# Performance work log

Hardware: AMD Instinct MI355X
Metric: run time of the kernel (lower is better)

The kernel has to match this reference:

```python
import jax, jax.numpy as jnp
import numpy as np

NUM_GRAPHS = 1024  # number of graphs in the batch (readout segments)


def setup_inputs() -> dict:
    key = jax.random.key(0)
    ks = jax.random.split(key, 10)
    N, F_IN, F1, F2, E = 100000, 64, 128, 64, 3200000
    x = jax.random.normal(ks[0], (N, F_IN), dtype=jnp.float32)
    adj = jax.random.randint(ks[1], (2, E), 0, N, dtype=jnp.int64)
    batch = jnp.sort(jax.random.randint(ks[2], (N,), 0, NUM_GRAPHS, dtype=jnp.int64))
    def xavier(k, shape):
        fan_in, fan_out = shape
        lim = jnp.sqrt(6.0 / (fan_in + fan_out))
        return jax.random.uniform(k, shape, jnp.float32, -lim, lim)
    W1 = xavier(ks[3], (F_IN, F1)); b1 = jax.random.uniform(ks[4], (F1,), jnp.float32)
    W2 = xavier(ks[5], (F1, F2));  b2 = jax.random.uniform(ks[6], (F2,), jnp.float32)
    Wm = xavier(ks[7], (2 * F2, F2)); bm = jax.random.uniform(ks[8], (F2,), jnp.float32)
    return {"x": x, "adj": adj, "batch": batch,
            "W1": W1, "b1": b1, "W2": W2, "b2": b2, "Wm": Wm, "bm": bm}


def _gcn_conv(x, W, b, src, dst):
    # GCNConv: out = D^{-1/2} (A + I) D^{-1/2} X W + b
    N = x.shape[0]
    h = x @ W  # [N, F_out]
    loops = jnp.arange(N, dtype=src.dtype)
    src_a = jnp.concatenate([src, loops])  # add self-loops
    dst_a = jnp.concatenate([dst, loops])
    deg = jax.ops.segment_sum(jnp.ones(src_a.shape[0], h.dtype), dst_a, num_segments=N)
    dinv = jax.lax.rsqrt(deg)  # deg >= 1 due to self-loops
    norm = dinv[src_a] * dinv[dst_a]  # [E+N]
    msg = h[src_a] * norm[:, None]    # gather + scale (memory-bound)
    return jax.ops.segment_sum(msg, dst_a, num_segments=N) + b


def _readout_meanmax(x, batch):
    G = NUM_GRAPHS
    s = jax.ops.segment_sum(x, batch, num_segments=G)
    cnt = jax.ops.segment_sum(jnp.ones(x.shape[0], x.dtype), batch, num_segments=G)
    mean = s / jnp.maximum(cnt, 1.0)[:, None]
    mx = jax.ops.segment_max(x, batch, num_segments=G)
    return jnp.concatenate([mean, mx], axis=1)  # [G, 2*F2]


def reference(x, adj, batch, W1, b1, W2, b2, Wm, bm):
    src, dst = adj[0], adj[1]
    h = jax.nn.relu(_gcn_conv(x, W1, b1, src, dst))
    h = _gcn_conv(h, W2, b2, src, dst)
    r = _readout_meanmax(h, batch)
    return r @ Wm + bm
```

## Files before the change

kernel.cpp:

```cpp
#include <hip/hip_runtime.h>
#include <hip/hip_fp16.h>
#include <cstdint>
#include <cstddef>

#define NGRAPH 1024
#define CHUNK 8192
#define SCTHREADS 512
#define SCIT (CHUNK / SCTHREADS)
#define MAXB 512
#define CAP 16384
#define WIDE 2048

typedef _Float16 f16x8 __attribute__((ext_vector_type(8)));
typedef float f32x4 __attribute__((ext_vector_type(4)));
typedef float f32x2 __attribute__((ext_vector_type(2)));


__global__ __launch_bounds__(SCTHREADS) void scatter1_kernel(const int* __restrict__ src,
        const int* __restrict__ dst, int E, int B,
        int* __restrict__ bcnt, unsigned* __restrict__ ebuck) {
    __shared__ unsigned sorted[CHUNK];
    __shared__ int h[MAXB];
    __shared__ int lo[MAXB];
    __shared__ int cur[MAXB];
    __shared__ int gbase[MAXB];
    __shared__ int wsum[8];
    int blk = blockIdx.x, tid = threadIdx.x;
    int base = blk * CHUNK;
    int cnt_i = E - base; if (cnt_i > CHUNK) cnt_i = CHUNK;

    h[tid] = 0;
    __syncthreads();

    unsigned rd[SCIT], rs[SCIT];
    #pragma unroll
    for (int it = 0; it < SCIT; ++it) {
        int i = base + tid + it * SCTHREADS;
        if (i < E) {
            rd[it] = (unsigned)dst[i];
            rs[it] = (unsigned)src[i];
            atomicAdd(&h[rd[it] >> 8], 1);
        } else rd[it] = 0xFFFFFFFFu;
    }
    __syncthreads();

    int hv = h[tid];
    if (tid < B) gbase[tid] = hv ? atomicAdd(&bcnt[tid], hv) : 0;

    int lane = tid & 63, wv = tid >> 6;
    int val = hv;
    #pragma unroll
    for (int o = 1; o < 64; o <<= 1) {
        int t = __shfl_up(val, o, 64);
        if (lane >= o) val += t;
    }
    if (lane == 63) wsum[wv] = val;
    __syncthreads();
    if (tid == 0) {
        int run = 0;
        #pragma unroll
        for (int i = 0; i < 8; ++i) { int t = wsum[i]; wsum[i] = run; run += t; }
    }
    __syncthreads();
    int excl = wsum[wv] + val - hv;
    lo[tid] = excl;
    cur[tid] = excl;
    __syncthreads();

    #pragma unroll
    for (int it = 0; it < SCIT; ++it) {
        if (rd[it] != 0xFFFFFFFFu) {
            int b = rd[it] >> 8;
            int p = atomicAdd(&cur[b], 1);
            sorted[p] = ((rd[it] & 255u) << 24) | rs[it];
        }
    }
    __syncthreads();

    for (int j = tid; j < cnt_i; j += SCTHREADS) {
        int l = (int)(((long long)j * B) / cnt_i);
        if (l > B - 1) l = B - 1;
        while (lo[l] > j) --l;
        while (l + 1 < B && lo[l + 1] <= j) ++l;
        ebuck[(size_t)l * CAP + gbase[l] + (j - lo[l])] = sorted[j];
    }
}

__global__ __launch_bounds__(256) void fine_kernel(const unsigned* __restrict__ ebuck,
        const int* __restrict__ bcnt, int N, int B,
        int* __restrict__ row_beg, int* __restrict__ row_end, float* __restrict__ dinv,
        int* __restrict__ esrc) {
    __shared__ int hcnt[256];
    __shared__ int loff[256];
    __shared__ int wsum[4];
    int b = blockIdx.x, tid = threadIdx.x;
    int beg = b * CAP;
    int cnt = bcnt[b];
    hcnt[tid] = 0;
    __syncthreads();
    {
        int e = tid;
        for (; e + 768 < cnt; e += 1024) {
            unsigned u0 = ebuck[beg + e];
            unsigned u1 = ebuck[beg + e + 256];
            unsigned u2 = ebuck[beg + e + 512];
            unsigned u3 = ebuck[beg + e + 768];
            atomicAdd(&hcnt[u0 >> 24], 1);
            atomicAdd(&hcnt[u1 >> 24], 1);
            atomicAdd(&hcnt[u2 >> 24], 1);
            atomicAdd(&hcnt[u3 >> 24], 1);
        }
        for (; e < cnt; e += 256)
            atomicAdd(&hcnt[ebuck[beg + e] >> 24], 1);
    }
    __syncthreads();
    int v = hcnt[tid];
    int n = (b << 8) + tid;
    int vp = (v + 15) & ~15;
    if (vp < 48) vp = 48;
    if (n >= N) vp = 0;

    int lane = tid & 63, wv = tid >> 6;
    int val = vp;
    #pragma unroll
    for (int o = 1; o < 64; o <<= 1) {
        int t = __shfl_up(val, o, 64);
        if (lane >= o) val += t;
    }
    if (lane == 63) wsum[wv] = val;
    __syncthreads();
    if (tid == 0) {
        int run = 0;
        #pragma unroll
        for (int i = 0; i < 4; ++i) { int t = wsum[i]; wsum[i] = run; run += t; }
    }
    __syncthreads();
    int excl = wsum[wv] + val - vp;

    float d = rsqrtf((float)(v + 1));
    if (n < N) {
        row_beg[n] = beg + excl;
        row_end[n] = beg + excl + vp;
        dinv[n] = d;
    }
    loff[tid] = excl;
    __syncthreads();
    {
        int e = tid;
        for (; e + 768 < cnt; e += 1024) {
            unsigned u0 = ebuck[beg + e];
            unsigned u1 = ebuck[beg + e + 256];
            unsigned u2 = ebuck[beg + e + 512];
            unsigned u3 = ebuck[beg + e + 768];
            int p0 = atomicAdd(&loff[u0 >> 24], 1);
            esrc[beg + p0] = (int)(u0 & 0xFFFFFF);
            int p1 = atomicAdd(&loff[u1 >> 24], 1);
            esrc[beg + p1] = (int)(u1 & 0xFFFFFF);
            int p2 = atomicAdd(&loff[u2 >> 24], 1);
            esrc[beg + p2] = (int)(u2 & 0xFFFFFF);
            int p3 = atomicAdd(&loff[u3 >> 24], 1);
            esrc[beg + p3] = (int)(u3 & 0xFFFFFF);
        }
        for (; e < cnt; e += 256) {
            unsigned u = ebuck[beg + e];
            int p = atomicAdd(&loff[u >> 24], 1);
            esrc[beg + p] = (int)(u & 0xFFFFFF);
        }
    }
    for (int p = excl + v; p < excl + vp; ++p) esrc[beg + p] = N;
}

__global__ __launch_bounds__(256) void pack_kernel(const float* __restrict__ x,
        const float* __restrict__ dinv, int N, unsigned char* __restrict__ xs) {
    int j = blockIdx.x * 256 + threadIdx.x;
    int total = N * 16;
    int stride = gridDim.x * 256;
    const float4* xr = (const float4*)x;
    for (; j < total; j += stride) {
        int node = j >> 4, cc = j & 15;
        float dd = dinv[node];
        float4 vv = xr[(size_t)node * 16 + cc];
        int lo2 = __builtin_amdgcn_cvt_pk_fp8_f32(vv.x * dd, vv.y * dd, 0, false);
        int hi2 = __builtin_amdgcn_cvt_pk_fp8_f32(vv.z * dd, vv.w * dd, 0, false);
        ((unsigned*)xs)[(size_t)node * 16 + cc] =
            (unsigned)(lo2 & 0xffff) | ((unsigned)(hi2 & 0xffff) << 16);
    }
}

__global__ __launch_bounds__(256) void prep_kernel(const float* __restrict__ W1,
        const float* __restrict__ W2, __half* __restrict__ W1s, __half* __restrict__ W2s,
        const int* __restrict__ batch, int N, int* __restrict__ goff,
        int* __restrict__ bcnt, unsigned char* __restrict__ xsq,
        unsigned char* __restrict__ tsq, float* __restrict__ zbias) {
    int t = threadIdx.x;
    if (blockIdx.x == 0) {
        #pragma unroll
        for (int it = 0; it < 4; ++it) {
            int s = t + it * 256;
            int n = s & 15, q = (s >> 4) & 3, nt = (s >> 6) & 7, ks = s >> 9;
            int k0 = ks * 32 + q * 8, col = nt * 16 + n;
            __align__(16) __half h[8];
            #pragma unroll
            for (int j = 0; j < 8; ++j) h[j] = (__half)W1[(k0 + j) * 128 + col];
            *((uint4*)&W1s[(size_t)s * 8]) = *(uint4*)h;
        }
        #pragma unroll
        for (int it = 0; it < 4; ++it) {
            int s = t + it * 256;
            int n = s & 15, q = (s >> 4) & 3, n2 = (s >> 6) & 3, ks2 = s >> 8;
            int k0 = ks2 * 32 + q * 8, col = n2 * 16 + n;
            __align__(16) __half h[8];
            #pragma unroll
            for (int j = 0; j < 8; ++j) h[j] = (__half)W2[(k0 + j) * 64 + col];
            *((uint4*)&W2s[(size_t)s * 8]) = *(uint4*)h;
        }
        uint4 z; z.x = 0; z.y = 0; z.z = 0; z.w = 0;
        if (t < 4)
            ((uint4*)(xsq + (size_t)N * 64))[t] = z;
        if (t < 4)
            ((uint4*)(tsq + (size_t)N * 64))[t] = z;
        if (t < 64) zbias[t] = 0.f;
    } else {
        int g = (blockIdx.x - 1) * 256 + t;
        if (g < MAXB) bcnt[g] = 0;
        if (g > NGRAPH) return;
        if (g == NGRAPH) { goff[g] = N; return; }
        int lo = 0, hi = N;
        while (lo < hi) {
            int mid = (lo + hi) >> 1;
            if (batch[mid] < g) lo = mid + 1; else hi = mid;
        }
        goff[g] = lo;
    }
}

__device__ __forceinline__ void acc8q(f32x2* a, const uint2& u) {
    a[0] += __builtin_amdgcn_cvt_pk_f32_fp8(u.x, false);
    a[1] += __builtin_amdgcn_cvt_pk_f32_fp8(u.x, true);
    a[2] += __builtin_amdgcn_cvt_pk_f32_fp8(u.y, false);
    a[3] += __builtin_amdgcn_cvt_pk_f32_fp8(u.y, true);
}

__device__ __forceinline__ void agg_core_q(const uint2* __restrict__ ts2,
        const int* __restrict__ esrc, int beg, int endp, int n, int g, int c,
        float* a) {
    f32x2 h0[4] = {}, h1[4] = {};
    if (g == 0) acc8q(h0, ts2[(size_t)n * 8 + c]);
    int U = (endp - beg) >> 3;
    int e0 = beg + g * U;
    if (U == 6) {
        int2 p0 = *(const int2*)&esrc[e0];
        int2 p1 = *(const int2*)&esrc[e0 + 2];
        int2 p2 = *(const int2*)&esrc[e0 + 4];
        uint2 u0 = ts2[(size_t)p0.x * 8 + c];
        uint2 u1 = ts2[(size_t)p0.y * 8 + c];
        uint2 u2 = ts2[(size_t)p1.x * 8 + c];
        uint2 u3 = ts2[(size_t)p1.y * 8 + c];
        uint2 u4 = ts2[(size_t)p2.x * 8 + c];
        uint2 u5 = ts2[(size_t)p2.y * 8 + c];
        acc8q(h0, u0); acc8q(h1, u1); acc8q(h0, u2); acc8q(h1, u3);
        acc8q(h0, u4); acc8q(h1, u5);
    } else if (U > 0) {
        for (int j = 0; j < U; j += 2) {
            int2 p = *(const int2*)&esrc[e0 + j];
            uint2 ua = ts2[(size_t)p.x * 8 + c];
            uint2 ub = ts2[(size_t)p.y * 8 + c];
            acc8q(h0, ua);
            acc8q(h1, ub);
        }
    }
    #pragma unroll
    for (int i = 0; i < 4; ++i) {
        a[2 * i]     = h0[i].x + h1[i].x;
        a[2 * i + 1] = h0[i].y + h1[i].y;
    }
}

__global__ __launch_bounds__(256) void agg_q2h_kernel(const unsigned char* __restrict__ ts,
        const int* __restrict__ esrc, const int* __restrict__ row_beg,
        const int* __restrict__ row_end, const float* __restrict__ dinv,
        const float* __restrict__ bias, __half* __restrict__ out, int N) {
    int n = blockIdx.x * 4 + (threadIdx.x >> 6);
    if (n >= N) return;
    int lane = threadIdx.x & 63;
    int g = lane >> 3, c = lane & 7;
    const uint2* ts2 = (const uint2*)ts;
    float a[8];
    agg_core_q(ts2, esrc, row_beg[n], row_end[n], n, g, c, a);
    #pragma unroll
    for (int i = 0; i < 8; ++i) {
        a[i] += __shfl_xor(a[i], 8, 64);
        a[i] += __shfl_xor(a[i], 16, 64);
        a[i] += __shfl_xor(a[i], 32, 64);
    }
    if (g == 0) {
        float d = dinv[n];
        float4 bb0 = ((const float4*)bias)[c * 2];
        float4 bb1 = ((const float4*)bias)[c * 2 + 1];
        __align__(16) __half2 h[4];
        h[0] = __floats2half2_rn(a[0] * d + bb0.x, a[1] * d + bb0.y);
        h[1] = __floats2half2_rn(a[2] * d + bb0.z, a[3] * d + bb0.w);
        h[2] = __floats2half2_rn(a[4] * d + bb1.x, a[5] * d + bb1.y);
        h[3] = __floats2half2_rn(a[6] * d + bb1.z, a[7] * d + bb1.w);
        ((uint4*)out)[(size_t)n * 8 + c] = *(uint4*)h;
    }
}

__global__ __launch_bounds__(256) void fusedmlp_kernel(const __half* __restrict__ A,
        const __half* __restrict__ W1s, const __half* __restrict__ W2s,
        const float* __restrict__ b1, const float* __restrict__ dinv,
        unsigned char* __restrict__ T, int N) {
    __shared__ __align__(16) __half h1t[4][16][136];
    int tid = threadIdx.x;
    int w = tid >> 6, lane = tid & 63;
    int n15 = lane & 15, q = lane >> 4;
    int base = blockIdx.x * 64 + w * 16;

    int m = base + n15; if (m >= N) m = N - 1;
    const uint4* Ar = (const uint4*)(A + (size_t)m * 64);
    uint4 ua0 = Ar[q];
    uint4 ua1 = Ar[4 + q];
    f16x8 a10 = *(f16x8*)&ua0;
    f16x8 a11 = *(f16x8*)&ua1;
    const uint4* W1f = (const uint4*)W1s;
    #pragma unroll
    for (int nt = 0; nt < 8; ++nt) {
        f32x4 c = {0.f, 0.f, 0.f, 0.f};
        uint4 ub0 = W1f[(nt * 4 + q) * 16 + n15];
        uint4 ub1 = W1f[((8 + nt) * 4 + q) * 16 + n15];
        c = __builtin_amdgcn_mfma_f32_16x16x32_f16(a10, *(f16x8*)&ub0, c, 0, 0, 0);
        c = __builtin_amdgcn_mfma_f32_16x16x32_f16(a11, *(f16x8*)&ub1, c, 0, 0, 0);
        float bv = b1[nt * 16 + n15];
        #pragma unroll
        for (int rr = 0; rr < 4; ++rr) {
            float hv = fmaxf(c[rr] + bv, 0.f);
            h1t[w][q * 4 + rr][nt * 16 + n15] = (__half)hv;
        }
    }
    __syncthreads();

    f16x8 a2[4];
    #pragma unroll
    for (int ks2 = 0; ks2 < 4; ++ks2)
        a2[ks2] = *(f16x8*)&h1t[w][n15][ks2 * 32 + q * 8];
    const uint4* W2f = (const uint4*)W2s;
    #pragma unroll
    for (int n2 = 0; n2 < 4; ++n2) {
        f32x4 c = {0.f, 0.f, 0.f, 0.f};
        #pragma unroll
        for (int ks2 = 0; ks2 < 4; ++ks2) {
            uint4 ub = W2f[((ks2 * 4 + n2) * 4 + q) * 16 + n15];
            c = __builtin_amdgcn_mfma_f32_16x16x32_f16(a2[ks2], *(f16x8*)&ub, c, 0, 0, 0);
        }
        #pragma unroll
        for (int rr = 0; rr < 4; ++rr) {
            int node = base + q * 4 + rr;
            if (node < N) {
                float v = c[rr] * dinv[node];
                int pk = __builtin_amdgcn_cvt_pk_fp8_f32(v, v, 0, false);
                T[(size_t)node * 64 + n2 * 16 + n15] = (unsigned char)(pk & 0xff);
            }
        }
    }
}

__global__ __launch_bounds__(256) void readout_head_kernel(const __half* __restrict__ h2,
        const int* __restrict__ goff, const float* __restrict__ Wm,
        const float* __restrict__ bm, float* __restrict__ out) {
    int g = blockIdx.x;
    int beg = goff[g], end = goff[g + 1];
    int f = threadIdx.x & 63;
    int c = threadIdx.x >> 6;
    float s = 0.f, m = -3.4e38f;
    for (int n = beg + c; n < end; n += 4) {
        float v = __half2float(h2[(size_t)n * 64 + f]);
        s += v;
        m = fmaxf(m, v);
    }
    __shared__ float ss[4][64], sm[4][64];
    __shared__ float rr[128];
    ss[c][f] = s; sm[c][f] = m;
    __syncthreads();
    if (c == 0) {
        float S = ss[0][f] + ss[1][f] + ss[2][f] + ss[3][f];
        float M = fmaxf(fmaxf(sm[0][f], sm[1][f]), fmaxf(sm[2][f], sm[3][f]));
        int cnt = end - beg;
        rr[f] = (cnt > 0) ? S / (float)cnt : 0.f;
        rr[64 + f] = (cnt > 0) ? M : 0.f;
    }
    __syncthreads();
    if (threadIdx.x < 64) {
        int j = threadIdx.x;
        float acc = bm[j];
        #pragma unroll 4
        for (int k = 0; k < 128; ++k)
            acc = fmaf(rr[k], Wm[k * 64 + j], acc);
        out[(size_t)g * 64 + j] = acc;
    }
}

extern "C" void kernel_launch(void* const* d_in, const int* in_sizes, int n_in,
                              void* d_out, int out_size, void* d_ws, size_t ws_size,
                              hipStream_t stream) {
    const float* x    = (const float*)d_in[0];
    const int*  adj   = (const int*)d_in[1];
    const int*  batch = (const int*)d_in[2];
    const float* W1   = (const float*)d_in[3];
    const float* b1   = (const float*)d_in[4];
    const float* W2   = (const float*)d_in[5];
    const float* b2   = (const float*)d_in[6];
    const float* Wm   = (const float*)d_in[7];
    const float* bm   = (const float*)d_in[8];
    float* out = (float*)d_out;

    const int N = in_sizes[0] / 64;
    const int E = in_sizes[1] / 2;
    const int* src = adj;
    const int* dst = adj + E;
    const int B = (N + 255) >> 8;
    const int nblocks = (E + CHUNK - 1) / CHUNK;

    char* w = (char*)d_ws;
    size_t off = 0;
    auto carve = [&](size_t bytes) -> void* {
        void* p = w + off;
        off += (bytes + 255) & ~(size_t)255;
        return p;
    };
    size_t halfbuf = (size_t)N * 64 * 2;
    float* dinv    = (float*)carve((size_t)N * 4);
    int*   row_beg = (int*)  carve((size_t)N * 4);
    int*   row_end = (int*)  carve((size_t)N * 4);
    int*   esrc    = (int*)  carve((size_t)B * CAP * 4);
    unsigned* ebuck= (unsigned*)carve((size_t)B * CAP * 4);
    int*   bcnt    = (int*)  carve((MAXB + 1) * 4);
    int*   goff    = (int*)  carve((NGRAPH + 1) * 4);
    __half* W1s    = (__half*)carve(8192 * 2);
    __half* W2s    = (__half*)carve(8192 * 2);
    unsigned char* xs_q = (unsigned char*)carve((size_t)N * 64 + 64);
    __half* agg1h  = (__half*)carve(halfbuf);
    __half* h2     = (__half*)carve(halfbuf);
    unsigned char* ts_q = (unsigned char*)carve((size_t)N * 64 + 64);
    float* zbias   = (float*)carve(256);

    prep_kernel<<<1 + (NGRAPH + 256) / 256, 256, 0, stream>>>(W1, W2, W1s, W2s,
                                                              batch, N, goff, bcnt,
                                                              xs_q, ts_q, zbias);

    scatter1_kernel<<<nblocks, SCTHREADS, 0, stream>>>(src, dst, E, B, bcnt, ebuck);
    fine_kernel<<<B, 256, 0, stream>>>(ebuck, bcnt, N, B, row_beg, row_end,
                                       dinv, esrc);

    pack_kernel<<<WIDE, 256, 0, stream>>>(x, dinv, N, xs_q);

    agg_q2h_kernel<<<(N + 3) / 4, 256, 0, stream>>>(xs_q, esrc, row_beg, row_end,
                                                    dinv, zbias, agg1h, N);

    fusedmlp_kernel<<<(N + 63) / 64, 256, 0, stream>>>(agg1h, W1s, W2s, b1, dinv, ts_q, N);

    agg_q2h_kernel<<<(N + 3) / 4, 256, 0, stream>>>(ts_q, esrc, row_beg, row_end,
                                                    dinv, b2, h2, N);

    readout_head_kernel<<<NGRAPH, 256, 0, stream>>>(h2, goff, Wm, bm, out);
}
```

Before: 271.6 us.

## Fuse first-layer aggregation with the two-layer MLP into one kernel

Merges the layer-1 aggregation kernel and the fused MLP kernel. Each 1024-thread block aggregates 16 nodes (one wave per node) into LDS, then four waves run the MFMA matmuls and write the FP8 transformed features. This removes the fp16 intermediate buffer's global write and read-back and one kernel launch. In exchange, 12 of the 16 waves sit idle during the MLP phase, and the two block-wide barriers with large blocks may reduce latency hiding for the gather.

Measured after the change: 281.8 us. 3.7% more time.

```diff
diff --git a/kernel.cpp b/kernel.cpp
--- a/kernel.cpp
+++ b/kernel.cpp
@@ -276,6 +276,92 @@
     }
 }
 
+__global__ __launch_bounds__(1024, 8) void agg1mlp_kernel(
+        const unsigned char* __restrict__ ts, const int* __restrict__ esrc,
+        const int* __restrict__ row_beg, const int* __restrict__ row_end,
+        const float* __restrict__ dinv, const __half* __restrict__ W1s,
+        const __half* __restrict__ W2s, const float* __restrict__ b1,
+        unsigned char* __restrict__ T, int N) {
+    __shared__ __align__(16) __half ldsA[16][72];
+    __shared__ __align__(16) __half h1t[16][136];
+    int tid = threadIdx.x;
+    int w = tid >> 6, lane = tid & 63;
+    int base = blockIdx.x * 16;
+    int n = base + w;
+    int g = lane >> 3, c = lane & 7;
+
+    if (n < N) {
+        const uint2* ts2 = (const uint2*)ts;
+        float a[8];
+        agg_core_q(ts2, esrc, row_beg[n], row_end[n], n, g, c, a);
+        #pragma unroll
+        for (int i = 0; i < 8; ++i) {
+            a[i] += __shfl_xor(a[i], 8, 64);
+            a[i] += __shfl_xor(a[i], 16, 64);
+            a[i] += __shfl_xor(a[i], 32, 64);
+        }
+        if (g == 0) {
+            float d = dinv[n];
+            __align__(16) __half2 h[4];
+            #pragma unroll
+            for (int i = 0; i < 4; ++i)
+                h[i] = __floats2half2_rn(a[2 * i] * d, a[2 * i + 1] * d);
+            ((uint4*)&ldsA[w][0])[c] = *(uint4*)h;
+        }
+    } else if (g == 0) {
+        uint4 z; z.x = 0; z.y = 0; z.z = 0; z.w = 0;
+        ((uint4*)&ldsA[w][0])[c] = z;
+    }
+    __syncthreads();
+
+    int n15 = lane & 15, q = lane >> 4;
+    if (w < 4) {
+        uint4 ua0 = ((const uint4*)&ldsA[n15][0])[q];
+        uint4 ua1 = ((const uint4*)&ldsA[n15][0])[4 + q];
+        f16x8 a10 = *(f16x8*)&ua0;
+        f16x8 a11 = *(f16x8*)&ua1;
+        const uint4* W1f = (const uint4*)W1s;
+        #pragma unroll
+        for (int j = 0; j < 2; ++j) {
+            int nt = w * 2 + j;
+            f32x4 cc = {0.f, 0.f, 0.f, 0.f};
+            uint4 ub0 = W1f[(nt * 4 + q) * 16 + n15];
+            uint4 ub1 = W1f[((8 + nt) * 4 + q) * 16 + n15];
+            cc = __builtin_amdgcn_mfma_f32_16x16x32_f16(a10, *(f16x8*)&ub0, cc, 0, 0, 0);
+            cc = __builtin_amdgcn_mfma_f32_16x16x32_f16(a11, *(f16x8*)&ub1, cc, 0, 0, 0);
+            float bv = b1[nt * 16 + n15];
+            #pragma unroll
+            for (int rr = 0; rr < 4; ++rr) {
+                float hv = fmaxf(cc[rr] + bv, 0.f);
+                h1t[q * 4 + rr][nt * 16 + n15] = (__half)hv;
+            }
+        }
+    }
+    __syncthreads();
+    if (w >= 4) return;
+
+    f16x8 a2[4];
+    #pragma unroll
+    for (int ks2 = 0; ks2 < 4; ++ks2)
+        a2[ks2] = *(f16x8*)&h1t[n15][ks2 * 32 + q * 8];
+    const uint4* W2f = (const uint4*)W2s;
+    f32x4 cc = {0.f, 0.f, 0.f, 0.f};
+    #pragma unroll
+    for (int ks2 = 0; ks2 < 4; ++ks2) {
+        uint4 ub = W2f[((ks2 * 4 + w) * 4 + q) * 16 + n15];
+        cc = __builtin_amdgcn_mfma_f32_16x16x32_f16(a2[ks2], *(f16x8*)&ub, cc, 0, 0, 0);
+    }
+    #pragma unroll
+    for (int rr = 0; rr < 4; ++rr) {
+        int node = base + q * 4 + rr;
+        if (node < N) {
+            float v = cc[rr] * dinv[node];
+            int pk = __builtin_amdgcn_cvt_pk_fp8_f32(v, v, 0, false);
+            T[(size_t)node * 64 + w * 16 + n15] = (unsigned char)(pk & 0xff);
+        }
+    }
+}
+
 __global__ __launch_bounds__(256) void agg_q2h_kernel(const unsigned char* __restrict__ ts,
         const int* __restrict__ esrc, const int* __restrict__ row_beg,
         const int* __restrict__ row_end, const float* __restrict__ dinv,
@@ -303,64 +389,6 @@
         h[2] = __floats2half2_rn(a[4] * d + bb1.x, a[5] * d + bb1.y);
         h[3] = __floats2half2_rn(a[6] * d + bb1.z, a[7] * d + bb1.w);
         ((uint4*)out)[(size_t)n * 8 + c] = *(uint4*)h;
-    }
-}
-
-__global__ __launch_bounds__(256) void fusedmlp_kernel(const __half* __restrict__ A,
-        const __half* __restrict__ W1s, const __half* __restrict__ W2s,
-        const float* __restrict__ b1, const float* __restrict__ dinv,
-        unsigned char* __restrict__ T, int N) {
-    __shared__ __align__(16) __half h1t[4][16][136];
-    int tid = threadIdx.x;
-    int w = tid >> 6, lane = tid & 63;
-    int n15 = lane & 15, q = lane >> 4;
-    int base = blockIdx.x * 64 + w * 16;
-
-    int m = base + n15; if (m >= N) m = N - 1;
-    const uint4* Ar = (const uint4*)(A + (size_t)m * 64);
-    uint4 ua0 = Ar[q];
-    uint4 ua1 = Ar[4 + q];
-    f16x8 a10 = *(f16x8*)&ua0;
-    f16x8 a11 = *(f16x8*)&ua1;
-    const uint4* W1f = (const uint4*)W1s;
-    #pragma unroll
-    for (int nt = 0; nt < 8; ++nt) {
-        f32x4 c = {0.f, 0.f, 0.f, 0.f};
-        uint4 ub0 = W1f[(nt * 4 + q) * 16 + n15];
-        uint4 ub1 = W1f[((8 + nt) * 4 + q) * 16 + n15];
-        c = __builtin_amdgcn_mfma_f32_16x16x32_f16(a10, *(f16x8*)&ub0, c, 0, 0, 0);
-        c = __builtin_amdgcn_mfma_f32_16x16x32_f16(a11, *(f16x8*)&ub1, c, 0, 0, 0);
-        float bv = b1[nt * 16 + n15];
-        #pragma unroll
-        for (int rr = 0; rr < 4; ++rr) {
-            float hv = fmaxf(c[rr] + bv, 0.f);
-            h1t[w][q * 4 + rr][nt * 16 + n15] = (__half)hv;
-        }
-    }
-    __syncthreads();
-
-    f16x8 a2[4];
-    #pragma unroll
-    for (int ks2 = 0; ks2 < 4; ++ks2)
-        a2[ks2] = *(f16x8*)&h1t[w][n15][ks2 * 32 + q * 8];
-    const uint4* W2f = (const uint4*)W2s;
-    #pragma unroll
-    for (int n2 = 0; n2 < 4; ++n2) {
-        f32x4 c = {0.f, 0.f, 0.f, 0.f};
-        #pragma unroll
-        for (int ks2 = 0; ks2 < 4; ++ks2) {
-            uint4 ub = W2f[((ks2 * 4 + n2) * 4 + q) * 16 + n15];
-            c = __builtin_amdgcn_mfma_f32_16x16x32_f16(a2[ks2], *(f16x8*)&ub, c, 0, 0, 0);
-        }
-        #pragma unroll
-        for (int rr = 0; rr < 4; ++rr) {
-            int node = base + q * 4 + rr;
-            if (node < N) {
-                float v = c[rr] * dinv[node];
-                int pk = __builtin_amdgcn_cvt_pk_fp8_f32(v, v, 0, false);
-                T[(size_t)node * 64 + n2 * 16 + n15] = (unsigned char)(pk & 0xff);
-            }
-        }
     }
 }
 
@@ -438,7 +466,6 @@
     __half* W1s    = (__half*)carve(8192 * 2);
     __half* W2s    = (__half*)carve(8192 * 2);
     unsigned char* xs_q = (unsigned char*)carve((size_t)N * 64 + 64);
-    __half* agg1h  = (__half*)carve(halfbuf);
     __half* h2     = (__half*)carve(halfbuf);
     unsigned char* ts_q = (unsigned char*)carve((size_t)N * 64 + 64);
     float* zbias   = (float*)carve(256);
@@ -453,10 +480,8 @@
 
     pack_kernel<<<WIDE, 256, 0, stream>>>(x, dinv, N, xs_q);
 
-    agg_q2h_kernel<<<(N + 3) / 4, 256, 0, stream>>>(xs_q, esrc, row_beg, row_end,
-                                                    dinv, zbias, agg1h, N);
-
-    fusedmlp_kernel<<<(N + 63) / 64, 256, 0, stream>>>(agg1h, W1s, W2s, b1, dinv, ts_q, N);
+    agg1mlp_kernel<<<(N + 15) / 16, 1024, 0, stream>>>(xs_q, esrc, row_beg, row_end,
+                                                       dinv, W1s, W2s, b1, ts_q, N);
 
     agg_q2h_kernel<<<(N + 3) / 4, 256, 0, stream>>>(ts_q, esrc, row_beg, row_end,
                                                     dinv, b2, h2, N);
```
